# Kernel optimization log

Measured on AMD Instinct MI355X. Metric: run time of the kernel, lower is better.

The kernel has to match this reference:

```python
import jax, jax.numpy as jnp
import numpy as np

N_WIRES = 10
DIM = 1 << N_WIRES  # 1024
EPS = 1e-12

_CNOT = jnp.array([[1, 0, 0, 0],
                   [0, 1, 0, 0],
                   [0, 0, 0, 1],
                   [0, 0, 1, 0]], dtype=jnp.complex64)

# signs[i, j] = (-1)^{bit_j(i)} for single-Z Pauli string on wire j (qubit 0 = MSB)
_bits = (np.arange(DIM)[:, None] >> (N_WIRES - 1 - np.arange(N_WIRES))[None, :]) & 1
_Z_SIGNS = jnp.asarray(1.0 - 2.0 * _bits, dtype=jnp.float32)  # (DIM, N_WIRES)


def _rx_gate(theta):
    c = jnp.cos(theta / 2).astype(jnp.complex64)
    s = jnp.sin(theta / 2).astype(jnp.complex64)
    return jnp.stack([jnp.stack([c, -1j * s]), jnp.stack([-1j * s, c])])


def _ry_gate(theta):
    c = jnp.cos(theta / 2).astype(jnp.complex64)
    s = jnp.sin(theta / 2).astype(jnp.complex64)
    return jnp.stack([jnp.stack([c, -s]), jnp.stack([s, c])])


def _apply_1q(psi, gate, q):
    # psi: (N, DIM) complex64; apply 2x2 gate on qubit q (qubit 0 = MSB)
    N = psi.shape[0]
    left, right = 1 << q, 1 << (N_WIRES - 1 - q)
    psi = psi.reshape(N, left, 2, right)
    psi = jnp.einsum('ab,nxby->nxay', gate, psi)
    return psi.reshape(N, DIM)


def _apply_2q(psi, gate, q0, q1):
    # gate: (4,4) acting on qubits (q0, q1) in that order
    G = gate.reshape(2, 2, 2, 2)
    if q0 > q1:
        G = jnp.transpose(G, (1, 0, 3, 2))
        q0, q1 = q1, q0
    N = psi.shape[0]
    a = 1 << q0
    b = 1 << (q1 - q0 - 1)
    c = 1 << (N_WIRES - 1 - q1)
    psi = psi.reshape(N, a, 2, b, 2, c)
    psi = jnp.einsum('ijkl,nxkylz->nxiyjz', G, psi)
    return psi.reshape(N, DIM)


def setup_inputs() -> dict:
    key = jax.random.key(0)
    k1, k2, k3, k4 = jax.random.split(key, 4)
    x = jax.random.normal(k1, (4, 1024, DIM), dtype=jnp.float32)
    rx0 = jax.random.normal(k2, (N_WIRES,), dtype=jnp.float32)
    ry0 = jax.random.normal(k3, (N_WIRES,), dtype=jnp.float32)
    ry1 = jax.random.normal(k4, (N_WIRES,), dtype=jnp.float32)
    return {"x": x, "rx0": rx0, "ry0": ry0, "ry1": ry1}


def reference(x, rx0, ry0, ry1):
    B, T, C = x.shape
    x_flat = x.reshape(B * T, C)
    # amplitude encoding: L2-normalize each row into a complex state vector
    norm = jnp.linalg.norm(x_flat, axis=1, keepdims=True)
    psi = (x_flat / jnp.maximum(norm, EPS)).astype(jnp.complex64)  # (N, DIM)
    # layer 1: RX then RY on each wire
    for j in range(N_WIRES):
        psi = _apply_1q(psi, _rx_gate(rx0[j]), j)
        psi = _apply_1q(psi, _ry_gate(ry0[j]), j)
    # CNOT ring
    for j in range(N_WIRES):
        psi = _apply_2q(psi, _CNOT, j, (j + 1) % N_WIRES)
    # layer 2: RY on each wire
    for j in range(N_WIRES):
        psi = _apply_1q(psi, _ry_gate(ry1[j]), j)
    # expectation values of Z on each wire: sum_i |psi_i|^2 * (-1)^{bit_j(i)}
    probs = psi.real ** 2 + psi.imag ** 2  # (N, DIM) float32
    out = probs @ _Z_SIGNS                  # (N, N_WIRES)
    return out.reshape(B, T, N_WIRES).astype(jnp.float32)
```

## Files before the change

kernel.cpp:

```cpp
#include <hip/hip_runtime.h>

#define NW   10
#define QDIM 1024

__device__ __host__ __forceinline__ int gperm(int v) {
    #pragma unroll
    for (int k = 9; k >= 0; --k) {
        const int cs = 9 - k;
        const int ts = 9 - ((k + 1) % NW);
        v ^= ((v >> cs) & 1) << ts;
    }
    return v;
}

__device__ __forceinline__ int P2i(int i) {
    return i + ((i >> 4) << 1) + ((i >> 8) << 1);
}

template<int SH>
__device__ __forceinline__ void cgates(float* re, float* im,
                                       float ar, float ai, float br, float bi) {
    #pragma unroll
    for (int base = 0; base < 16; base += (2 << SH)) {
        #pragma unroll
        for (int off = 0; off < (1 << SH); ++off) {
            const int r0 = base + off, r1 = r0 + (1 << SH);
            const float v0r = re[r0], v0i = im[r0];
            const float v1r = re[r1], v1i = im[r1];
            re[r0] =  ar * v0r - ai * v0i + br * v1r - bi * v1i;
            im[r0] =  ar * v0i + ai * v0r + br * v1i + bi * v1r;
            re[r1] = -br * v0r - bi * v0i + ar * v1r + ai * v1i;
            im[r1] =  bi * v0r - br * v0i + ar * v1i - ai * v1r;
        }
    }
}

template<int SH>
__device__ __forceinline__ void rgates(float* re, float* im, float c, float s) {
    #pragma unroll
    for (int base = 0; base < 16; base += (2 << SH)) {
        #pragma unroll
        for (int off = 0; off < (1 << SH); ++off) {
            const int r0 = base + off, r1 = r0 + (1 << SH);
            const float v0r = re[r0], v0i = im[r0];
            const float v1r = re[r1], v1i = im[r1];
            re[r0] = c * v0r - s * v1r;  im[r0] = c * v0i - s * v1i;
            re[r1] = s * v0r + c * v1r;  im[r1] = s * v0i + c * v1i;
        }
    }
}

__global__ void qsa_coef(const float* __restrict__ rx0,
                         const float* __restrict__ ry0,
                         const float* __restrict__ ry1,
                         float* __restrict__ cf) {
    const int j = threadIdx.x;
    if (j < NW) {
        float sx, cx, sy0, cy0, sy1, cy1;
        sincosf(0.5f * rx0[j], &sx,  &cx);
        sincosf(0.5f * ry0[j], &sy0, &cy0);
        sincosf(0.5f * ry1[j], &sy1, &cy1);
        cf[4 * j + 0] =  cy0 * cx;
        cf[4 * j + 1] =  sy0 * sx;
        cf[4 * j + 2] = -sy0 * cx;
        cf[4 * j + 3] = -cy0 * sx;
        cf[40 + 2 * j]     = cy1;
        cf[40 + 2 * j + 1] = sy1;
    }
}

__global__ __launch_bounds__(64) void qsa_main(
    const float* __restrict__ x,
    const float* __restrict__ cf,
    float* __restrict__ out) {

    __shared__ __align__(16) float2 sp[1160];

    const int t = threadIdx.x;
    const int n = blockIdx.x;

    float g1[40], g2[20];
    #pragma unroll
    for (int k = 0; k < 40; ++k) g1[k] = cf[k];
    #pragma unroll
    for (int k = 0; k < 20; ++k) g2[k] = cf[40 + k];

    float re[16], im[16];
    const float* xr = x + ((size_t)n << 10) + (t << 4);
    float ss = 0.f;
    #pragma unroll
    for (int r = 0; r < 16; r += 4) {
        const float4 v = *reinterpret_cast<const float4*>(xr + r);
        re[r] = v.x; re[r + 1] = v.y; re[r + 2] = v.z; re[r + 3] = v.w;
        ss += v.x * v.x + v.y * v.y + v.z * v.z + v.w * v.w;
    }
    #pragma unroll
    for (int off = 32; off > 0; off >>= 1) ss += __shfl_xor(ss, off, 64);
    const float scale = 1.0f / fmaxf(sqrtf(ss), 1e-12f);

    {
        const float ar = g1[36], ai = g1[37], br = g1[38], bi = g1[39];
        #pragma unroll
        for (int r = 0; r < 16; r += 2) {
            const float v0 = re[r] * scale, v1 = re[r + 1] * scale;
            re[r]     =  ar * v0 + br * v1;  im[r]     = ai * v0 + bi * v1;
            re[r + 1] = -br * v0 + ar * v1;  im[r + 1] = bi * v0 - ai * v1;
        }
    }
    cgates<1>(re, im, g1[32], g1[33], g1[34], g1[35]);
    cgates<2>(re, im, g1[28], g1[29], g1[30], g1[31]);
    cgates<3>(re, im, g1[24], g1[25], g1[26], g1[27]);

    #pragma unroll
    for (int r = 0; r < 16; r += 2) {
        const int i = (t << 4) | r;
        *reinterpret_cast<float4*>(&sp[P2i(i)]) =
            make_float4(re[r], im[r], re[r + 1], im[r + 1]);
    }
    __syncthreads();
    {
        const int hi = (t >> 4) << 8, lo = t & 15;
        #pragma unroll
        for (int r = 0; r < 16; ++r) {
            const float2 v = sp[P2i(hi | (r << 4) | lo)];
            re[r] = v.x; im[r] = v.y;
        }
    }

    cgates<0>(re, im, g1[20], g1[21], g1[22], g1[23]);
    cgates<1>(re, im, g1[16], g1[17], g1[18], g1[19]);
    cgates<2>(re, im, g1[12], g1[13], g1[14], g1[15]);
    cgates<3>(re, im, g1[ 8], g1[ 9], g1[10], g1[11]);

    __syncthreads();
    {
        const int hi = (t >> 4) << 8, lo = t & 15;
        #pragma unroll
        for (int r = 0; r < 16; ++r)
            sp[P2i(hi | (r << 4) | lo)] = make_float2(re[r], im[r]);
    }
    __syncthreads();
    #pragma unroll
    for (int r = 0; r < 16; r += 2) {
        const int i = (((r >> 2) & 3) << 8) | (t << 2) | (r & 3);
        const float4 v = *reinterpret_cast<const float4*>(&sp[P2i(i)]);
        re[r] = v.x; im[r] = v.y; re[r + 1] = v.z; im[r + 1] = v.w;
    }

    cgates<2>(re, im, g1[4], g1[5], g1[6], g1[7]);
    cgates<3>(re, im, g1[0], g1[1], g1[2], g1[3]);

    __syncthreads();
    #pragma unroll
    for (int r = 0; r < 16; r += 2) {
        const int i = (((r >> 2) & 3) << 8) | (t << 2) | (r & 3);
        *reinterpret_cast<float4*>(&sp[P2i(i)]) =
            make_float4(re[r], im[r], re[r + 1], im[r + 1]);
    }
    __syncthreads();
    {
        const int gt = gperm(t << 4);
        #pragma unroll
        for (int r = 0; r < 16; ++r) {
            const float2 v = sp[P2i(gt ^ gperm(r))];
            re[r] = v.x; im[r] = v.y;
        }
    }

    rgates<0>(re, im, g2[18], g2[19]);
    rgates<1>(re, im, g2[16], g2[17]);
    rgates<2>(re, im, g2[14], g2[15]);
    rgates<3>(re, im, g2[12], g2[13]);

    __syncthreads();
    #pragma unroll
    for (int r = 0; r < 16; r += 2) {
        const int i = (t << 4) | r;
        *reinterpret_cast<float4*>(&sp[P2i(i)]) =
            make_float4(re[r], im[r], re[r + 1], im[r + 1]);
    }
    __syncthreads();
    {
        const int hi = (t >> 4) << 8, lo = t & 15;
        #pragma unroll
        for (int r = 0; r < 16; ++r) {
            const float2 v = sp[P2i(hi | (r << 4) | lo)];
            re[r] = v.x; im[r] = v.y;
        }
    }

    rgates<0>(re, im, g2[10], g2[11]);
    rgates<1>(re, im, g2[ 8], g2[ 9]);
    rgates<2>(re, im, g2[ 6], g2[ 7]);
    rgates<3>(re, im, g2[ 4], g2[ 5]);

    __syncthreads();
    {
        const int hi = (t >> 4) << 8, lo = t & 15;
        #pragma unroll
        for (int r = 0; r < 16; ++r)
            sp[P2i(hi | (r << 4) | lo)] = make_float2(re[r], im[r]);
    }
    __syncthreads();
    #pragma unroll
    for (int r = 0; r < 16; r += 2) {
        const int i = (((r >> 2) & 3) << 8) | (t << 2) | (r & 3);
        const float4 v = *reinterpret_cast<const float4*>(&sp[P2i(i)]);
        re[r] = v.x; im[r] = v.y; re[r + 1] = v.z; im[r + 1] = v.w;
    }

    rgates<2>(re, im, g2[2], g2[3]);
    rgates<3>(re, im, g2[0], g2[1]);

    float sj[6];
    #pragma unroll
    for (int j = 2; j < 8; ++j)
        sj[j - 2] = 1.0f - 2.0f * (float)((t >> (7 - j)) & 1);

    float acc[NW];
    #pragma unroll
    for (int j = 0; j < NW; ++j) acc[j] = 0.f;

    #pragma unroll
    for (int r = 0; r < 16; ++r) {
        const float p = re[r] * re[r] + im[r] * im[r];
        if (r & 8) acc[0] -= p; else acc[0] += p;
        if (r & 4) acc[1] -= p; else acc[1] += p;
        if (r & 2) acc[8] -= p; else acc[8] += p;
        if (r & 1) acc[9] -= p; else acc[9] += p;
        #pragma unroll
        for (int j = 2; j < 8; ++j) acc[j] = fmaf(sj[j - 2], p, acc[j]);
    }

    #pragma unroll
    for (int j = 0; j < NW; ++j) {
        #pragma unroll
        for (int off = 32; off > 0; off >>= 1)
            acc[j] += __shfl_xor(acc[j], off, 64);
    }
    if (t == 0) {
        #pragma unroll
        for (int j = 0; j < NW; ++j) out[(size_t)n * NW + j] = acc[j];
    }
}

extern "C" void kernel_launch(void* const* d_in, const int* in_sizes, int n_in,
                              void* d_out, int out_size, void* d_ws, size_t ws_size,
                              hipStream_t stream) {
    const float* x   = (const float*)d_in[0];
    const float* rx0 = (const float*)d_in[1];
    const float* ry0 = (const float*)d_in[2];
    const float* ry1 = (const float*)d_in[3];
    float* out = (float*)d_out;
    float* cf  = (float*)d_ws;
    const int nstates = in_sizes[0] / QDIM;

    qsa_coef<<<1, 64, 0, stream>>>(rx0, ry0, ry1, cf);
    qsa_main<<<nstates, 64, 0, stream>>>(x, cf, out);
}
```

Measured before the change: 85.87 us.

## Process two states per block with 32 amplitudes per thread and fewer transposes

Each 64-thread block now handles two state vectors, one per half-wavefront, and each thread holds 32 amplitudes instead of 16. This cuts the number of shared-memory transpose rounds from four to three, with the CNOT permutation folded into one of them. The final Z-expectation reduction now uses a butterfly that produces all signed sums together, replacing ten separate full reductions. The cost is higher register pressure (64 floats of state per thread), which may lower occupancy or cause spills, and the launch assumes an even number of states.

```diff
diff --git a/kernel.cpp b/kernel.cpp
--- a/kernel.cpp
+++ b/kernel.cpp
@@ -2,8 +2,9 @@
 
 #define NW   10
 #define QDIM 1024
-
-__device__ __host__ __forceinline__ int gperm(int v) {
+#define SBUF 1160
+
+__device__ __forceinline__ int gperm(int v) {
     #pragma unroll
     for (int k = 9; k >= 0; --k) {
         const int cs = 9 - k;
@@ -13,15 +14,13 @@
     return v;
 }
 
-__device__ __forceinline__ int P2i(int i) {
-    return i + ((i >> 4) << 1) + ((i >> 8) << 1);
-}
+__device__ __forceinline__ int P2i(int i) { return i + ((i >> 4) << 1); }
 
 template<int SH>
-__device__ __forceinline__ void cgates(float* re, float* im,
-                                       float ar, float ai, float br, float bi) {
-    #pragma unroll
-    for (int base = 0; base < 16; base += (2 << SH)) {
+__device__ __forceinline__ void cg32(float* re, float* im,
+                                     float ar, float ai, float br, float bi) {
+    #pragma unroll
+    for (int base = 0; base < 32; base += (2 << SH)) {
         #pragma unroll
         for (int off = 0; off < (1 << SH); ++off) {
             const int r0 = base + off, r1 = r0 + (1 << SH);
@@ -36,9 +35,9 @@
 }
 
 template<int SH>
-__device__ __forceinline__ void rgates(float* re, float* im, float c, float s) {
-    #pragma unroll
-    for (int base = 0; base < 16; base += (2 << SH)) {
+__device__ __forceinline__ void rg32(float* re, float* im, float c, float s) {
+    #pragma unroll
+    for (int base = 0; base < 32; base += (2 << SH)) {
         #pragma unroll
         for (int off = 0; off < (1 << SH); ++off) {
             const int r0 = base + off, r1 = r0 + (1 << SH);
@@ -74,10 +73,13 @@
     const float* __restrict__ cf,
     float* __restrict__ out) {
 
-    __shared__ __align__(16) float2 sp[1160];
-
-    const int t = threadIdx.x;
-    const int n = blockIdx.x;
+    __shared__ __align__(16) float2 sp[2 * SBUF];
+
+    const int t   = threadIdx.x;
+    const int s   = t & 31;
+    const int sub = t >> 5;
+    const int n   = (blockIdx.x << 1) | sub;
+    float2* mysp  = sp + sub * SBUF;
 
     float g1[40], g2[20];
     #pragma unroll
@@ -85,163 +87,116 @@
     #pragma unroll
     for (int k = 0; k < 20; ++k) g2[k] = cf[40 + k];
 
-    float re[16], im[16];
-    const float* xr = x + ((size_t)n << 10) + (t << 4);
+    float re[32], im[32];
+    const float* xr = x + ((size_t)n << 10) + (s << 5);
     float ss = 0.f;
     #pragma unroll
-    for (int r = 0; r < 16; r += 4) {
+    for (int r = 0; r < 32; r += 4) {
         const float4 v = *reinterpret_cast<const float4*>(xr + r);
         re[r] = v.x; re[r + 1] = v.y; re[r + 2] = v.z; re[r + 3] = v.w;
         ss += v.x * v.x + v.y * v.y + v.z * v.z + v.w * v.w;
     }
     #pragma unroll
-    for (int off = 32; off > 0; off >>= 1) ss += __shfl_xor(ss, off, 64);
+    for (int b = 16; b > 0; b >>= 1) ss += __shfl_xor(ss, b, 64);
     const float scale = 1.0f / fmaxf(sqrtf(ss), 1e-12f);
 
     {
         const float ar = g1[36], ai = g1[37], br = g1[38], bi = g1[39];
         #pragma unroll
-        for (int r = 0; r < 16; r += 2) {
+        for (int r = 0; r < 32; r += 2) {
             const float v0 = re[r] * scale, v1 = re[r + 1] * scale;
             re[r]     =  ar * v0 + br * v1;  im[r]     = ai * v0 + bi * v1;
             re[r + 1] = -br * v0 + ar * v1;  im[r + 1] = bi * v0 - ai * v1;
         }
     }
-    cgates<1>(re, im, g1[32], g1[33], g1[34], g1[35]);
-    cgates<2>(re, im, g1[28], g1[29], g1[30], g1[31]);
-    cgates<3>(re, im, g1[24], g1[25], g1[26], g1[27]);
-
-    #pragma unroll
-    for (int r = 0; r < 16; r += 2) {
-        const int i = (t << 4) | r;
-        *reinterpret_cast<float4*>(&sp[P2i(i)]) =
+    cg32<1>(re, im, g1[32], g1[33], g1[34], g1[35]);
+    cg32<2>(re, im, g1[28], g1[29], g1[30], g1[31]);
+    cg32<3>(re, im, g1[24], g1[25], g1[26], g1[27]);
+    cg32<4>(re, im, g1[20], g1[21], g1[22], g1[23]);
+
+    #pragma unroll
+    for (int r = 0; r < 32; r += 2)
+        *reinterpret_cast<float4*>(&mysp[P2i((s << 5) | r)]) =
             make_float4(re[r], im[r], re[r + 1], im[r + 1]);
-    }
+    __syncthreads();
+    #pragma unroll
+    for (int r = 0; r < 32; ++r) {
+        const float2 v = mysp[P2i((r << 5) | s)];
+        re[r] = v.x; im[r] = v.y;
+    }
+
+    cg32<0>(re, im, g1[16], g1[17], g1[18], g1[19]);
+    cg32<1>(re, im, g1[12], g1[13], g1[14], g1[15]);
+    cg32<2>(re, im, g1[ 8], g1[ 9], g1[10], g1[11]);
+    cg32<3>(re, im, g1[ 4], g1[ 5], g1[ 6], g1[ 7]);
+    cg32<4>(re, im, g1[ 0], g1[ 1], g1[ 2], g1[ 3]);
+
+    __syncthreads();
+    #pragma unroll
+    for (int r = 0; r < 32; ++r)
+        mysp[P2i((r << 5) | s)] = make_float2(re[r], im[r]);
     __syncthreads();
     {
-        const int hi = (t >> 4) << 8, lo = t & 15;
-        #pragma unroll
-        for (int r = 0; r < 16; ++r) {
-            const float2 v = sp[P2i(hi | (r << 4) | lo)];
+        const int gt = gperm(s << 5);
+        #pragma unroll
+        for (int r = 0; r < 32; ++r) {
+            const float2 v = mysp[P2i(gt ^ gperm(r))];
             re[r] = v.x; im[r] = v.y;
         }
     }
 
-    cgates<0>(re, im, g1[20], g1[21], g1[22], g1[23]);
-    cgates<1>(re, im, g1[16], g1[17], g1[18], g1[19]);
-    cgates<2>(re, im, g1[12], g1[13], g1[14], g1[15]);
-    cgates<3>(re, im, g1[ 8], g1[ 9], g1[10], g1[11]);
-
-    __syncthreads();
-    {
-        const int hi = (t >> 4) << 8, lo = t & 15;
-        #pragma unroll
-        for (int r = 0; r < 16; ++r)
-            sp[P2i(hi | (r << 4) | lo)] = make_float2(re[r], im[r]);
-    }
-    __syncthreads();
-    #pragma unroll
-    for (int r = 0; r < 16; r += 2) {
-        const int i = (((r >> 2) & 3) << 8) | (t << 2) | (r & 3);
-        const float4 v = *reinterpret_cast<const float4*>(&sp[P2i(i)]);
-        re[r] = v.x; im[r] = v.y; re[r + 1] = v.z; im[r + 1] = v.w;
-    }
-
-    cgates<2>(re, im, g1[4], g1[5], g1[6], g1[7]);
-    cgates<3>(re, im, g1[0], g1[1], g1[2], g1[3]);
-
-    __syncthreads();
-    #pragma unroll
-    for (int r = 0; r < 16; r += 2) {
-        const int i = (((r >> 2) & 3) << 8) | (t << 2) | (r & 3);
-        *reinterpret_cast<float4*>(&sp[P2i(i)]) =
+    rg32<0>(re, im, g2[18], g2[19]);
+    rg32<1>(re, im, g2[16], g2[17]);
+    rg32<2>(re, im, g2[14], g2[15]);
+    rg32<3>(re, im, g2[12], g2[13]);
+    rg32<4>(re, im, g2[10], g2[11]);
+
+    __syncthreads();
+    #pragma unroll
+    for (int r = 0; r < 32; r += 2)
+        *reinterpret_cast<float4*>(&mysp[P2i((s << 5) | r)]) =
             make_float4(re[r], im[r], re[r + 1], im[r + 1]);
-    }
-    __syncthreads();
-    {
-        const int gt = gperm(t << 4);
-        #pragma unroll
-        for (int r = 0; r < 16; ++r) {
-            const float2 v = sp[P2i(gt ^ gperm(r))];
-            re[r] = v.x; im[r] = v.y;
-        }
-    }
-
-    rgates<0>(re, im, g2[18], g2[19]);
-    rgates<1>(re, im, g2[16], g2[17]);
-    rgates<2>(re, im, g2[14], g2[15]);
-    rgates<3>(re, im, g2[12], g2[13]);
-
-    __syncthreads();
-    #pragma unroll
-    for (int r = 0; r < 16; r += 2) {
-        const int i = (t << 4) | r;
-        *reinterpret_cast<float4*>(&sp[P2i(i)]) =
-            make_float4(re[r], im[r], re[r + 1], im[r + 1]);
-    }
-    __syncthreads();
-    {
-        const int hi = (t >> 4) << 8, lo = t & 15;
-        #pragma unroll
-        for (int r = 0; r < 16; ++r) {
-            const float2 v = sp[P2i(hi | (r << 4) | lo)];
-            re[r] = v.x; im[r] = v.y;
-        }
-    }
-
-    rgates<0>(re, im, g2[10], g2[11]);
-    rgates<1>(re, im, g2[ 8], g2[ 9]);
-    rgates<2>(re, im, g2[ 6], g2[ 7]);
-    rgates<3>(re, im, g2[ 4], g2[ 5]);
-
-    __syncthreads();
-    {
-        const int hi = (t >> 4) << 8, lo = t & 15;
-        #pragma unroll
-        for (int r = 0; r < 16; ++r)
-            sp[P2i(hi | (r << 4) | lo)] = make_float2(re[r], im[r]);
-    }
-    __syncthreads();
-    #pragma unroll
-    for (int r = 0; r < 16; r += 2) {
-        const int i = (((r >> 2) & 3) << 8) | (t << 2) | (r & 3);
-        const float4 v = *reinterpret_cast<const float4*>(&sp[P2i(i)]);
-        re[r] = v.x; im[r] = v.y; re[r + 1] = v.z; im[r + 1] = v.w;
-    }
-
-    rgates<2>(re, im, g2[2], g2[3]);
-    rgates<3>(re, im, g2[0], g2[1]);
-
-    float sj[6];
-    #pragma unroll
-    for (int j = 2; j < 8; ++j)
-        sj[j - 2] = 1.0f - 2.0f * (float)((t >> (7 - j)) & 1);
-
-    float acc[NW];
-    #pragma unroll
-    for (int j = 0; j < NW; ++j) acc[j] = 0.f;
-
-    #pragma unroll
-    for (int r = 0; r < 16; ++r) {
+    __syncthreads();
+    #pragma unroll
+    for (int r = 0; r < 32; ++r) {
+        const float2 v = mysp[P2i((r << 5) | s)];
+        re[r] = v.x; im[r] = v.y;
+    }
+
+    rg32<0>(re, im, g2[ 8], g2[ 9]);
+    rg32<1>(re, im, g2[ 6], g2[ 7]);
+    rg32<2>(re, im, g2[ 4], g2[ 5]);
+    rg32<3>(re, im, g2[ 2], g2[ 3]);
+    rg32<4>(re, im, g2[ 0], g2[ 1]);
+
+    float P = 0.f, a0 = 0.f, a1 = 0.f, a2 = 0.f, a3 = 0.f, a4 = 0.f;
+    #pragma unroll
+    for (int r = 0; r < 32; ++r) {
         const float p = re[r] * re[r] + im[r] * im[r];
-        if (r & 8) acc[0] -= p; else acc[0] += p;
-        if (r & 4) acc[1] -= p; else acc[1] += p;
-        if (r & 2) acc[8] -= p; else acc[8] += p;
-        if (r & 1) acc[9] -= p; else acc[9] += p;
-        #pragma unroll
-        for (int j = 2; j < 8; ++j) acc[j] = fmaf(sj[j - 2], p, acc[j]);
-    }
-
-    #pragma unroll
-    for (int j = 0; j < NW; ++j) {
-        #pragma unroll
-        for (int off = 32; off > 0; off >>= 1)
-            acc[j] += __shfl_xor(acc[j], off, 64);
-    }
-    if (t == 0) {
-        #pragma unroll
-        for (int j = 0; j < NW; ++j) out[(size_t)n * NW + j] = acc[j];
-    }
+        P  += p;
+        a0 += (r & 16) ? -p : p;
+        a1 += (r &  8) ? -p : p;
+        a2 += (r &  4) ? -p : p;
+        a3 += (r &  2) ? -p : p;
+        a4 += (r &  1) ? -p : p;
+    }
+    #pragma unroll
+    for (int b = 1; b < 32; b <<= 1) {
+        a0 += __shfl_xor(a0, b, 64);
+        a1 += __shfl_xor(a1, b, 64);
+        a2 += __shfl_xor(a2, b, 64);
+        a3 += __shfl_xor(a3, b, 64);
+        a4 += __shfl_xor(a4, b, 64);
+        const float e = __shfl_xor(P, b, 64);
+        P = (s & b) ? (e - P) : (e + P);
+    }
+    float* o = out + (size_t)n * NW;
+    if (s == 0) { o[0] = a0; o[1] = a1; o[2] = a2; o[3] = a3; o[4] = a4; }
+    if (s == 1)  o[9] = P;
+    if (s == 2)  o[8] = P;
+    if (s == 4)  o[7] = P;
+    if (s == 8)  o[6] = P;
+    if (s == 16) o[5] = P;
 }
 
 extern "C" void kernel_launch(void* const* d_in, const int* in_sizes, int n_in,
@@ -256,5 +211,5 @@
     const int nstates = in_sizes[0] / QDIM;
 
     qsa_coef<<<1, 64, 0, stream>>>(rx0, ry0, ry1, cf);
-    qsa_main<<<nstates, 64, 0, stream>>>(x, cf, out);
-}
+    qsa_main<<<nstates / 2, 64, 0, stream>>>(x, cf, out);
+}
```

Result: slower. 93.62 us (+9.0%).

## Fuse coefficient kernel into main, split LDS re/im planes, use butterfly reduction

Applied to the files above, without the earlier changes.

Removes the separate coefficient kernel launch and has each block compute its gate sincos values into shared memory. The shared buffer is split into separate real and imaginary planes with a new padding function, and some barriers between read and write phases are dropped. The final Z-expectation reduction uses a butterfly that yields the six middle-wire sums via sign-flipping shuffles instead of reducing ten accumulators. The per-block sincos work is redundant across blocks but removes one launch and the global coefficient traffic.

```diff
diff --git a/kernel.cpp b/kernel.cpp
--- a/kernel.cpp
+++ b/kernel.cpp
@@ -1,9 +1,8 @@
 #include <hip/hip_runtime.h>
 
-#define NW   10
-#define QDIM 1024
-
-__device__ __host__ __forceinline__ int gperm(int v) {
+#define NW 10
+
+__device__ __forceinline__ int gperm(int v) {
     #pragma unroll
     for (int k = 9; k >= 0; --k) {
         const int cs = 9 - k;
@@ -13,13 +12,14 @@
     return v;
 }
 
-__device__ __forceinline__ int P2i(int i) {
-    return i + ((i >> 4) << 1) + ((i >> 8) << 1);
-}
+__device__ __forceinline__ int PF(int i) {
+    return i + ((i >> 5) << 2) + ((i >> 8) << 3);
+}
+#define PBUF 1176
 
 template<int SH>
-__device__ __forceinline__ void cgates(float* re, float* im,
-                                       float ar, float ai, float br, float bi) {
+__device__ __forceinline__ void cg(float* re, float* im,
+                                   float ar, float ai, float br, float bi) {
     #pragma unroll
     for (int base = 0; base < 16; base += (2 << SH)) {
         #pragma unroll
@@ -36,7 +36,7 @@
 }
 
 template<int SH>
-__device__ __forceinline__ void rgates(float* re, float* im, float c, float s) {
+__device__ __forceinline__ void rg(float* re, float* im, float c, float s) {
     #pragma unroll
     for (int base = 0; base < 16; base += (2 << SH)) {
         #pragma unroll
@@ -50,40 +50,32 @@
     }
 }
 
-__global__ void qsa_coef(const float* __restrict__ rx0,
-                         const float* __restrict__ ry0,
-                         const float* __restrict__ ry1,
-                         float* __restrict__ cf) {
-    const int j = threadIdx.x;
-    if (j < NW) {
-        float sx, cx, sy0, cy0, sy1, cy1;
-        sincosf(0.5f * rx0[j], &sx,  &cx);
-        sincosf(0.5f * ry0[j], &sy0, &cy0);
-        sincosf(0.5f * ry1[j], &sy1, &cy1);
-        cf[4 * j + 0] =  cy0 * cx;
-        cf[4 * j + 1] =  sy0 * sx;
-        cf[4 * j + 2] = -sy0 * cx;
-        cf[4 * j + 3] = -cy0 * sx;
-        cf[40 + 2 * j]     = cy1;
-        cf[40 + 2 * j + 1] = sy1;
-    }
-}
-
 __global__ __launch_bounds__(64) void qsa_main(
     const float* __restrict__ x,
-    const float* __restrict__ cf,
+    const float* __restrict__ rx0,
+    const float* __restrict__ ry0,
+    const float* __restrict__ ry1,
     float* __restrict__ out) {
 
-    __shared__ __align__(16) float2 sp[1160];
+    __shared__ __align__(16) float reb[PBUF];
+    __shared__ __align__(16) float imb[PBUF];
+    __shared__ float cf[64];
 
     const int t = threadIdx.x;
     const int n = blockIdx.x;
 
-    float g1[40], g2[20];
-    #pragma unroll
-    for (int k = 0; k < 40; ++k) g1[k] = cf[k];
-    #pragma unroll
-    for (int k = 0; k < 20; ++k) g2[k] = cf[40 + k];
+    if (t < NW) {
+        float sx, cx, sy0, cy0, sy1, cy1;
+        sincosf(0.5f * rx0[t], &sx,  &cx);
+        sincosf(0.5f * ry0[t], &sy0, &cy0);
+        sincosf(0.5f * ry1[t], &sy1, &cy1);
+        cf[4 * t + 0] =  cy0 * cx;
+        cf[4 * t + 1] =  sy0 * sx;
+        cf[4 * t + 2] = -sy0 * cx;
+        cf[4 * t + 3] = -cy0 * sx;
+        cf[40 + 2 * t]     = cy1;
+        cf[40 + 2 * t + 1] = sy1;
+    }
 
     float re[16], im[16];
     const float* xr = x + ((size_t)n << 10) + (t << 4);
@@ -95,11 +87,13 @@
         ss += v.x * v.x + v.y * v.y + v.z * v.z + v.w * v.w;
     }
     #pragma unroll
-    for (int off = 32; off > 0; off >>= 1) ss += __shfl_xor(ss, off, 64);
+    for (int b = 32; b > 0; b >>= 1) ss += __shfl_xor(ss, b, 64);
     const float scale = 1.0f / fmaxf(sqrtf(ss), 1e-12f);
 
-    {
-        const float ar = g1[36], ai = g1[37], br = g1[38], bi = g1[39];
+    __syncthreads();
+
+    {
+        const float ar = cf[36], ai = cf[37], br = cf[38], bi = cf[39];
         #pragma unroll
         for (int r = 0; r < 16; r += 2) {
             const float v0 = re[r] * scale, v1 = re[r + 1] * scale;
@@ -107,141 +101,142 @@
             re[r + 1] = -br * v0 + ar * v1;  im[r + 1] = bi * v0 - ai * v1;
         }
     }
-    cgates<1>(re, im, g1[32], g1[33], g1[34], g1[35]);
-    cgates<2>(re, im, g1[28], g1[29], g1[30], g1[31]);
-    cgates<3>(re, im, g1[24], g1[25], g1[26], g1[27]);
-
-    #pragma unroll
-    for (int r = 0; r < 16; r += 2) {
-        const int i = (t << 4) | r;
-        *reinterpret_cast<float4*>(&sp[P2i(i)]) =
-            make_float4(re[r], im[r], re[r + 1], im[r + 1]);
-    }
-    __syncthreads();
-    {
-        const int hi = (t >> 4) << 8, lo = t & 15;
-        #pragma unroll
-        for (int r = 0; r < 16; ++r) {
-            const float2 v = sp[P2i(hi | (r << 4) | lo)];
-            re[r] = v.x; im[r] = v.y;
-        }
-    }
-
-    cgates<0>(re, im, g1[20], g1[21], g1[22], g1[23]);
-    cgates<1>(re, im, g1[16], g1[17], g1[18], g1[19]);
-    cgates<2>(re, im, g1[12], g1[13], g1[14], g1[15]);
-    cgates<3>(re, im, g1[ 8], g1[ 9], g1[10], g1[11]);
-
-    __syncthreads();
-    {
-        const int hi = (t >> 4) << 8, lo = t & 15;
-        #pragma unroll
-        for (int r = 0; r < 16; ++r)
-            sp[P2i(hi | (r << 4) | lo)] = make_float2(re[r], im[r]);
-    }
-    __syncthreads();
-    #pragma unroll
-    for (int r = 0; r < 16; r += 2) {
-        const int i = (((r >> 2) & 3) << 8) | (t << 2) | (r & 3);
-        const float4 v = *reinterpret_cast<const float4*>(&sp[P2i(i)]);
-        re[r] = v.x; im[r] = v.y; re[r + 1] = v.z; im[r + 1] = v.w;
-    }
-
-    cgates<2>(re, im, g1[4], g1[5], g1[6], g1[7]);
-    cgates<3>(re, im, g1[0], g1[1], g1[2], g1[3]);
-
-    __syncthreads();
-    #pragma unroll
-    for (int r = 0; r < 16; r += 2) {
-        const int i = (((r >> 2) & 3) << 8) | (t << 2) | (r & 3);
-        *reinterpret_cast<float4*>(&sp[P2i(i)]) =
-            make_float4(re[r], im[r], re[r + 1], im[r + 1]);
+    cg<1>(re, im, cf[32], cf[33], cf[34], cf[35]);
+    cg<2>(re, im, cf[28], cf[29], cf[30], cf[31]);
+    cg<3>(re, im, cf[24], cf[25], cf[26], cf[27]);
+
+    #pragma unroll
+    for (int r = 0; r < 16; r += 4) {
+        const int p = PF((t << 4) + r);
+        *reinterpret_cast<float4*>(&reb[p]) = make_float4(re[r], re[r+1], re[r+2], re[r+3]);
+        *reinterpret_cast<float4*>(&imb[p]) = make_float4(im[r], im[r+1], im[r+2], im[r+3]);
+    }
+    __syncthreads();
+    {
+        const int b0 = ((t >> 4) << 8) | (t & 15);
+        #pragma unroll
+        for (int r = 0; r < 16; ++r) {
+            const int p = PF(b0 + (r << 4));
+            re[r] = reb[p]; im[r] = imb[p];
+        }
+    }
+
+    cg<0>(re, im, cf[20], cf[21], cf[22], cf[23]);
+    cg<1>(re, im, cf[16], cf[17], cf[18], cf[19]);
+    cg<2>(re, im, cf[12], cf[13], cf[14], cf[15]);
+    cg<3>(re, im, cf[ 8], cf[ 9], cf[10], cf[11]);
+
+    {
+        const int b0 = ((t >> 4) << 8) | (t & 15);
+        #pragma unroll
+        for (int r = 0; r < 16; ++r) {
+            const int p = PF(b0 + (r << 4));
+            reb[p] = re[r]; imb[p] = im[r];
+        }
+    }
+    __syncthreads();
+    #pragma unroll
+    for (int r = 0; r < 16; r += 4) {
+        const int p = PF(((r >> 2) << 8) | (t << 2));
+        float4 q = *reinterpret_cast<const float4*>(&reb[p]);
+        re[r] = q.x; re[r+1] = q.y; re[r+2] = q.z; re[r+3] = q.w;
+        q = *reinterpret_cast<const float4*>(&imb[p]);
+        im[r] = q.x; im[r+1] = q.y; im[r+2] = q.z; im[r+3] = q.w;
+    }
+
+    cg<2>(re, im, cf[4], cf[5], cf[6], cf[7]);
+    cg<3>(re, im, cf[0], cf[1], cf[2], cf[3]);
+
+    #pragma unroll
+    for (int r = 0; r < 16; r += 4) {
+        const int p = PF(((r >> 2) << 8) | (t << 2));
+        *reinterpret_cast<float4*>(&reb[p]) = make_float4(re[r], re[r+1], re[r+2], re[r+3]);
+        *reinterpret_cast<float4*>(&imb[p]) = make_float4(im[r], im[r+1], im[r+2], im[r+3]);
     }
     __syncthreads();
     {
         const int gt = gperm(t << 4);
         #pragma unroll
         for (int r = 0; r < 16; ++r) {
-            const float2 v = sp[P2i(gt ^ gperm(r))];
-            re[r] = v.x; im[r] = v.y;
-        }
-    }
-
-    rgates<0>(re, im, g2[18], g2[19]);
-    rgates<1>(re, im, g2[16], g2[17]);
-    rgates<2>(re, im, g2[14], g2[15]);
-    rgates<3>(re, im, g2[12], g2[13]);
-
-    __syncthreads();
-    #pragma unroll
-    for (int r = 0; r < 16; r += 2) {
-        const int i = (t << 4) | r;
-        *reinterpret_cast<float4*>(&sp[P2i(i)]) =
-            make_float4(re[r], im[r], re[r + 1], im[r + 1]);
-    }
-    __syncthreads();
-    {
-        const int hi = (t >> 4) << 8, lo = t & 15;
-        #pragma unroll
-        for (int r = 0; r < 16; ++r) {
-            const float2 v = sp[P2i(hi | (r << 4) | lo)];
-            re[r] = v.x; im[r] = v.y;
-        }
-    }
-
-    rgates<0>(re, im, g2[10], g2[11]);
-    rgates<1>(re, im, g2[ 8], g2[ 9]);
-    rgates<2>(re, im, g2[ 6], g2[ 7]);
-    rgates<3>(re, im, g2[ 4], g2[ 5]);
-
-    __syncthreads();
-    {
-        const int hi = (t >> 4) << 8, lo = t & 15;
-        #pragma unroll
-        for (int r = 0; r < 16; ++r)
-            sp[P2i(hi | (r << 4) | lo)] = make_float2(re[r], im[r]);
-    }
-    __syncthreads();
-    #pragma unroll
-    for (int r = 0; r < 16; r += 2) {
-        const int i = (((r >> 2) & 3) << 8) | (t << 2) | (r & 3);
-        const float4 v = *reinterpret_cast<const float4*>(&sp[P2i(i)]);
-        re[r] = v.x; im[r] = v.y; re[r + 1] = v.z; im[r + 1] = v.w;
-    }
-
-    rgates<2>(re, im, g2[2], g2[3]);
-    rgates<3>(re, im, g2[0], g2[1]);
-
-    float sj[6];
-    #pragma unroll
-    for (int j = 2; j < 8; ++j)
-        sj[j - 2] = 1.0f - 2.0f * (float)((t >> (7 - j)) & 1);
-
-    float acc[NW];
-    #pragma unroll
-    for (int j = 0; j < NW; ++j) acc[j] = 0.f;
-
+            const int p = PF(gt ^ gperm(r));
+            re[r] = reb[p]; im[r] = imb[p];
+        }
+    }
+
+    rg<0>(re, im, cf[58], cf[59]);
+    rg<1>(re, im, cf[56], cf[57]);
+    rg<2>(re, im, cf[54], cf[55]);
+    rg<3>(re, im, cf[52], cf[53]);
+
+    #pragma unroll
+    for (int r = 0; r < 16; r += 4) {
+        const int p = PF((t << 4) + r);
+        *reinterpret_cast<float4*>(&reb[p]) = make_float4(re[r], re[r+1], re[r+2], re[r+3]);
+        *reinterpret_cast<float4*>(&imb[p]) = make_float4(im[r], im[r+1], im[r+2], im[r+3]);
+    }
+    __syncthreads();
+    {
+        const int b0 = ((t >> 4) << 8) | (t & 15);
+        #pragma unroll
+        for (int r = 0; r < 16; ++r) {
+            const int p = PF(b0 + (r << 4));
+            re[r] = reb[p]; im[r] = imb[p];
+        }
+    }
+
+    rg<0>(re, im, cf[50], cf[51]);
+    rg<1>(re, im, cf[48], cf[49]);
+    rg<2>(re, im, cf[46], cf[47]);
+    rg<3>(re, im, cf[44], cf[45]);
+
+    {
+        const int b0 = ((t >> 4) << 8) | (t & 15);
+        #pragma unroll
+        for (int r = 0; r < 16; ++r) {
+            const int p = PF(b0 + (r << 4));
+            reb[p] = re[r]; imb[p] = im[r];
+        }
+    }
+    __syncthreads();
+    #pragma unroll
+    for (int r = 0; r < 16; r += 4) {
+        const int p = PF(((r >> 2) << 8) | (t << 2));
+        float4 q = *reinterpret_cast<const float4*>(&reb[p]);
+        re[r] = q.x; re[r+1] = q.y; re[r+2] = q.z; re[r+3] = q.w;
+        q = *reinterpret_cast<const float4*>(&imb[p]);
+        im[r] = q.x; im[r+1] = q.y; im[r+2] = q.z; im[r+3] = q.w;
+    }
+
+    rg<2>(re, im, cf[42], cf[43]);
+    rg<3>(re, im, cf[40], cf[41]);
+
+    float P = 0.f, a0 = 0.f, a1 = 0.f, a8 = 0.f, a9 = 0.f;
     #pragma unroll
     for (int r = 0; r < 16; ++r) {
         const float p = re[r] * re[r] + im[r] * im[r];
-        if (r & 8) acc[0] -= p; else acc[0] += p;
-        if (r & 4) acc[1] -= p; else acc[1] += p;
-        if (r & 2) acc[8] -= p; else acc[8] += p;
-        if (r & 1) acc[9] -= p; else acc[9] += p;
-        #pragma unroll
-        for (int j = 2; j < 8; ++j) acc[j] = fmaf(sj[j - 2], p, acc[j]);
-    }
-
-    #pragma unroll
-    for (int j = 0; j < NW; ++j) {
-        #pragma unroll
-        for (int off = 32; off > 0; off >>= 1)
-            acc[j] += __shfl_xor(acc[j], off, 64);
-    }
-    if (t == 0) {
-        #pragma unroll
-        for (int j = 0; j < NW; ++j) out[(size_t)n * NW + j] = acc[j];
-    }
+        P  += p;
+        a0 += (r & 8) ? -p : p;
+        a1 += (r & 4) ? -p : p;
+        a8 += (r & 2) ? -p : p;
+        a9 += (r & 1) ? -p : p;
+    }
+    #pragma unroll
+    for (int b = 1; b < 64; b <<= 1) {
+        a0 += __shfl_xor(a0, b, 64);
+        a1 += __shfl_xor(a1, b, 64);
+        a8 += __shfl_xor(a8, b, 64);
+        a9 += __shfl_xor(a9, b, 64);
+        const float e = __shfl_xor(P, b, 64);
+        P = (t & b) ? (e - P) : (e + P);
+    }
+    float* o = out + (size_t)n * NW;
+    if (t == 0) { o[0] = a0; o[1] = a1; o[8] = a8; o[9] = a9; }
+    if (t == 32) o[2] = P;
+    if (t == 16) o[3] = P;
+    if (t ==  8) o[4] = P;
+    if (t ==  4) o[5] = P;
+    if (t ==  2) o[6] = P;
+    if (t ==  1) o[7] = P;
 }
 
 extern "C" void kernel_launch(void* const* d_in, const int* in_sizes, int n_in,
@@ -252,9 +247,6 @@
     const float* ry0 = (const float*)d_in[2];
     const float* ry1 = (const float*)d_in[3];
     float* out = (float*)d_out;
-    float* cf  = (float*)d_ws;
-    const int nstates = in_sizes[0] / QDIM;
-
-    qsa_coef<<<1, 64, 0, stream>>>(rx0, ry0, ry1, cf);
-    qsa_main<<<nstates, 64, 0, stream>>>(x, cf, out);
-}
+    const int nstates = in_sizes[0] >> 10;
+    qsa_main<<<nstates, 64, 0, stream>>>(x, rx0, ry0, ry1, out);
+}
```

After: 82.35 us. -4.1%, faster.
